# Kernel optimization log

Measured on AMD Instinct MI355X. Metric: run time of the kernel, lower is better.

Reference implementation:

```python
import jax, jax.numpy as jnp
import numpy as np

OUT_H = OUT_W = 15      # POOLER_RESOLUTION (template / pooler_z path)
SCALE = 0.0625          # POOLER_SCALES: 1/16 feature stride
SR = 2                  # POOLER_SAMPLING_RATIO
IMG = 1024.0


def setup_inputs() -> dict:
    key = jax.random.key(0)
    k1, k2, k3, k4, k5 = jax.random.split(key, 5)
    x = jax.random.normal(k1, (2, 256, 64, 64), dtype=jnp.float32)
    N = 512
    cx = jax.random.uniform(k2, (N,), minval=32.0, maxval=IMG - 32.0)
    cy = jax.random.uniform(k3, (N,), minval=32.0, maxval=IMG - 32.0)
    wh = jax.random.uniform(k4, (N, 2), minval=32.0, maxval=160.0)
    x1 = jnp.clip(cx - wh[:, 0] / 2, 0.0, IMG - 1)
    x2 = jnp.clip(cx + wh[:, 0] / 2, 0.0, IMG - 1)
    y1 = jnp.clip(cy - wh[:, 1] / 2, 0.0, IMG - 1)
    y2 = jnp.clip(cy + wh[:, 1] / 2, 0.0, IMG - 1)
    boxes = jnp.stack([x1, y1, x2, y2], axis=1).astype(jnp.float32)
    batch_idx = jax.random.randint(k5, (N,), 0, 2, dtype=jnp.int32)
    return {"x": x, "boxes": boxes, "batch_idx": batch_idx}


def _axis_idx(p, size):
    """ROIAlign bilinear index/frac/validity along one axis. p: [N, K] float."""
    valid = (p >= -1.0) & (p <= size)
    p = jnp.clip(p, 0.0, size - 1.0)
    lo = jnp.floor(p).astype(jnp.int32)
    lo = jnp.minimum(lo, size - 1)
    hi = jnp.minimum(lo + 1, size - 1)
    frac = p - lo.astype(p.dtype)  # 0 when lo==size-1 (matches torch clamp)
    return lo, hi, frac, valid


def roi_align(feats, boxes, batch_idx, out_h, out_w, scale, sr):
    B, C, H, W = feats.shape
    b = boxes * scale
    x1, y1, x2, y2 = b[:, 0], b[:, 1], b[:, 2], b[:, 3]
    roi_w = jnp.maximum(x2 - x1, 1.0)
    roi_h = jnp.maximum(y2 - y1, 1.0)
    bin_w = roi_w / out_w
    bin_h = roi_h / out_h
    # sample point k along an axis: start + (k + 0.5)/sr * bin  (k = ph*sr + iy)
    ky = (jnp.arange(out_h * sr, dtype=feats.dtype) + 0.5) / sr
    kx = (jnp.arange(out_w * sr, dtype=feats.dtype) + 0.5) / sr
    ys = y1[:, None] + ky[None, :] * bin_h[:, None]  # [N, out_h*sr]
    xs = x1[:, None] + kx[None, :] * bin_w[:, None]  # [N, out_w*sr]
    ylo, yhi, fy, vy = _axis_idx(ys, H)
    xlo, xhi, fx, vx = _axis_idx(xs, W)
    bi = batch_idx[:, None, None]

    def gather(yi, xi):
        # feats[b, :, y, x] -> [N, out_h*sr, out_w*sr, C]
        return feats[bi, :, yi[:, :, None], xi[:, None, :]]

    wy_lo = (1.0 - fy) * vy
    wy_hi = fy * vy
    wx_lo = (1.0 - fx) * vx
    wx_hi = fx * vx

    def w2(wy, wx):
        return (wy[:, :, None] * wx[:, None, :])[..., None]  # [N,Hs,Ws,1]

    val = (w2(wy_lo, wx_lo) * gather(ylo, xlo)
           + w2(wy_lo, wx_hi) * gather(ylo, xhi)
           + w2(wy_hi, wx_lo) * gather(yhi, xlo)
           + w2(wy_hi, wx_hi) * gather(yhi, xhi))
    N = boxes.shape[0]
    val = val.reshape(N, out_h, sr, out_w, sr, C).mean(axis=(2, 4))
    return jnp.transpose(val, (0, 3, 1, 2))  # [N, C, out_h, out_w]


def reference(x, boxes, batch_idx):
    # EMMFeatureExtractor.forward with sr=None -> pooler_z (template ROIAlign 15x15)
    return roi_align(x, boxes, batch_idx, OUT_H, OUT_W, SCALE, SR)
```

## Files before the change

kernel.cpp:

```cpp
#include <hip/hip_runtime.h>

constexpr int NROI = 512;
constexpr int CCH  = 256;
constexpr int HH   = 64;
constexpr int WWd  = 64;
constexpr int OHh  = 15;
constexpr int OWw  = 15;
constexpr float SCL = 0.0625f;
constexpr int TSTR  = 17;
constexpr int TROWS = 16;
constexpr int CHUNK  = 64;
constexpr int NCHUNK = CCH / CHUNK;

__global__ __launch_bounds__(256, 4)
void roi_align_kernel(const float* __restrict__ x,
                      const float* __restrict__ boxes,
                      const int* __restrict__ bidx,
                      float* __restrict__ out) {
  __shared__ float T[4][TROWS * TSTR];
  __shared__ float wx_s[OWw][3];
  __shared__ float wy_s[OHh][3];
  __shared__ int   jb_s[OWw];
  __shared__ int   rb_s[OHh];

  const int roi = blockIdx.x >> 2;
  const int g   = blockIdx.x & 3;
  const int t   = threadIdx.x;

  if (t < 32) {
    const int axis = t >> 4;
    const int o    = t & 15;
    if (o < OHh) {
      const float p1v = boxes[roi * 4 + axis] * SCL;
      const float p2v = boxes[roi * 4 + 2 + axis] * SCL;
      const float sz  = fmaxf(p2v - p1v, 1.0f);
      const float bin = sz * (1.0f / 15.0f);
      int lo[2]; float wl[2], wh[2];
#pragma unroll
      for (int s = 0; s < 2; ++s) {
        float p = p1v + ((float)(2 * o + s) + 0.5f) * 0.5f * bin;
        const float valid = (p >= -1.0f && p <= 64.0f) ? 0.5f : 0.0f;
        p = fminf(fmaxf(p, 0.0f), 63.0f);
        const int l = (int)p;
        const float f = p - (float)l;
        lo[s] = l; wl[s] = (1.0f - f) * valid; wh[s] = f * valid;
      }
      const int base = min(lo[0], WWd - 3);
      float w[3] = {0.f, 0.f, 0.f};
#pragma unroll
      for (int s = 0; s < 2; ++s) {
        const int hi = min(lo[s] + 1, WWd - 1);
        w[lo[s] - base] += wl[s];
        w[hi - base]    += wh[s];
      }
      if (axis == 0) { jb_s[o] = base; wx_s[o][0] = w[0]; wx_s[o][1] = w[1]; wx_s[o][2] = w[2]; }
      else           { rb_s[o] = base; wy_s[o][0] = w[0]; wy_s[o][1] = w[1]; wy_s[o][2] = w[2]; }
    }
  }
  __syncthreads();

  const int r0 = rb_s[0];
  const int R  = rb_s[OHh - 1] + 3 - r0;
  const int bi = bidx[roi];

  const bool hasA = (t < R * OWw);
  float ax0 = 0.f, ax1 = 0.f, ax2 = 0.f;
  const float* aptr = x;
  int aT = 0;
  if (hasA) {
    const int ar = t / OWw, aw = t - ar * OWw;
    ax0 = wx_s[aw][0]; ax1 = wx_s[aw][1]; ax2 = wx_s[aw][2];
    aptr = x + (((size_t)bi * CCH + g * CHUNK) * HH + (size_t)(r0 + ar)) * WWd + jb_s[aw];
    aT = ar * TSTR + aw;
  }

  const bool hasB = (t < OHh * OWw);
  float by0 = 0.f, by1 = 0.f, by2 = 0.f;
  int bT = 0;
  float* optr = out;
  if (hasB) {
    const int oh = t / OWw;
    by0 = wy_s[oh][0]; by1 = wy_s[oh][1]; by2 = wy_s[oh][2];
    bT = (rb_s[oh] - r0) * TSTR + (t - oh * OWw);
    optr = out + ((size_t)roi * CCH + (size_t)g * CHUNK) * (OHh * OWw) + t;
  }

  constexpr size_t CSTR = (size_t)HH * WWd;
  constexpr int OSTR = OHh * OWw;

  for (int it = 0; it < CHUNK / 2; ++it) {
    float* T0 = T[(it & 1) * 2];
    float* T1 = T[(it & 1) * 2 + 1];
    if (hasA) {
      const float* p0 = aptr;
      const float* p1 = aptr + CSTR;
      const float v0 = fmaf(p0[0], ax0, fmaf(p0[1], ax1, p0[2] * ax2));
      const float v1 = fmaf(p1[0], ax0, fmaf(p1[1], ax1, p1[2] * ax2));
      T0[aT] = v0;
      T1[aT] = v1;
      aptr += 2 * CSTR;
    }
    __syncthreads();
    if (hasB) {
      const float a0 = T0[bT], a1 = T0[bT + TSTR], a2 = T0[bT + 2 * TSTR];
      const float b0 = T1[bT], b1 = T1[bT + TSTR], b2 = T1[bT + 2 * TSTR];
      const float o0 = fmaf(a0, by0, fmaf(a1, by1, a2 * by2));
      const float o1 = fmaf(b0, by0, fmaf(b1, by1, b2 * by2));
      __builtin_nontemporal_store(o0, optr);
      __builtin_nontemporal_store(o1, optr + OSTR);
      optr += 2 * OSTR;
    }
  }
}

extern "C" void kernel_launch(void* const* d_in, const int* in_sizes, int n_in,
                              void* d_out, int out_size, void* d_ws, size_t ws_size,
                              hipStream_t stream) {
  const float* x     = (const float*)d_in[0];
  const float* boxes = (const float*)d_in[1];
  const int*   bid   = (const int*)d_in[2];
  float* out = (float*)d_out;
  hipLaunchKernelGGL(roi_align_kernel, dim3(NROI * NCHUNK), dim3(256), 0, stream,
                     x, boxes, bid, out);
}
```

Baseline: 156.6 us.

## Replace LDS two-stage separable ROIAlign with per-thread 2x2 register tiles

Drops the shared-memory staging and the per-iteration block barrier. Each lane now computes its own axis weights and produces a 2x2 tile of output bins from a 4x4 input window, read with four unaligned float4 loads per channel. The four waves each take 16 channels of the 64-channel chunk. This removes synchronization and LDS traffic but duplicates weight computation per thread. Edge lanes also write the same clamped outputs twice, and the non-temporal store hint is gone.

```diff
diff --git a/kernel.cpp b/kernel.cpp
--- a/kernel.cpp
+++ b/kernel.cpp
@@ -7,109 +7,112 @@
 constexpr int OHh  = 15;
 constexpr int OWw  = 15;
 constexpr float SCL = 0.0625f;
-constexpr int TSTR  = 17;
-constexpr int TROWS = 16;
 constexpr int CHUNK  = 64;
 constexpr int NCHUNK = CCH / CHUNK;
+constexpr int OSTR   = OHh * OWw;
+constexpr size_t CSTR = (size_t)HH * WWd;
+
+typedef float f4 __attribute__((ext_vector_type(4)));
+typedef f4 __attribute__((aligned(4))) f4a;
+
+__device__ __forceinline__ void axis_w(float p1v, float p2v, int o,
+                                       int& base, float& W0, float& W1, float& W2) {
+  const float sz  = fmaxf(p2v - p1v, 1.0f);
+  const float bin = sz * (1.0f / 15.0f);
+  float w0 = 0.f, w1 = 0.f, w2 = 0.f;
+  int l0 = 0;
+#pragma unroll
+  for (int s = 0; s < 2; ++s) {
+    float p = p1v + ((float)(2 * o + s) + 0.5f) * 0.5f * bin;
+    const float valid = (p >= -1.0f && p <= 64.0f) ? 0.5f : 0.0f;
+    p = fminf(fmaxf(p, 0.0f), 63.0f);
+    const int l = (int)p;
+    const float f = p - (float)l;
+    const float wl = (1.0f - f) * valid;
+    const float wh = f * valid;
+    if (s == 0) l0 = min(l, WWd - 3);
+    const int dl = l - l0;
+    const int dh = min(l + 1, WWd - 1) - l0;
+    w0 += (dl == 0) ? wl : 0.f;
+    w1 += (dl == 1) ? wl : 0.f;
+    w2 += (dl == 2) ? wl : 0.f;
+    w0 += (dh == 0) ? wh : 0.f;
+    w1 += (dh == 1) ? wh : 0.f;
+    w2 += (dh == 2) ? wh : 0.f;
+  }
+  base = l0; W0 = w0; W1 = w1; W2 = w2;
+}
+
+__device__ __forceinline__ f4 shift_w(float w0, float w1, float w2, int off) {
+  f4 r;
+  if (off == 0) { r.x = w0;  r.y = w1; r.z = w2; r.w = 0.f; }
+  else          { r.x = 0.f; r.y = w0; r.z = w1; r.w = w2;  }
+  return r;
+}
+
+__device__ __forceinline__ float dot4(f4 a, f4 w) {
+  return fmaf(a.x, w.x, fmaf(a.y, w.y, fmaf(a.z, w.z, a.w * w.w)));
+}
 
 __global__ __launch_bounds__(256, 4)
 void roi_align_kernel(const float* __restrict__ x,
                       const float* __restrict__ boxes,
                       const int* __restrict__ bidx,
                       float* __restrict__ out) {
-  __shared__ float T[4][TROWS * TSTR];
-  __shared__ float wx_s[OWw][3];
-  __shared__ float wy_s[OHh][3];
-  __shared__ int   jb_s[OWw];
-  __shared__ int   rb_s[OHh];
+  const int roi  = blockIdx.x >> 2;
+  const int g    = blockIdx.x & 3;
+  const int t    = threadIdx.x;
+  const int wv   = t >> 6;
+  const int lane = t & 63;
+  const int ohp  = lane >> 3;
+  const int owp  = lane & 7;
+  const int oh0 = min(2 * ohp, OHh - 2), oh1 = oh0 + 1;
+  const int ow0 = min(2 * owp, OWw - 2), ow1 = ow0 + 1;
 
-  const int roi = blockIdx.x >> 2;
-  const int g   = blockIdx.x & 3;
-  const int t   = threadIdx.x;
+  const float bx1 = boxes[roi * 4 + 0] * SCL;
+  const float by1 = boxes[roi * 4 + 1] * SCL;
+  const float bx2 = boxes[roi * 4 + 2] * SCL;
+  const float by2 = boxes[roi * 4 + 3] * SCL;
 
-  if (t < 32) {
-    const int axis = t >> 4;
-    const int o    = t & 15;
-    if (o < OHh) {
-      const float p1v = boxes[roi * 4 + axis] * SCL;
-      const float p2v = boxes[roi * 4 + 2 + axis] * SCL;
-      const float sz  = fmaxf(p2v - p1v, 1.0f);
-      const float bin = sz * (1.0f / 15.0f);
-      int lo[2]; float wl[2], wh[2];
-#pragma unroll
-      for (int s = 0; s < 2; ++s) {
-        float p = p1v + ((float)(2 * o + s) + 0.5f) * 0.5f * bin;
-        const float valid = (p >= -1.0f && p <= 64.0f) ? 0.5f : 0.0f;
-        p = fminf(fmaxf(p, 0.0f), 63.0f);
-        const int l = (int)p;
-        const float f = p - (float)l;
-        lo[s] = l; wl[s] = (1.0f - f) * valid; wh[s] = f * valid;
-      }
-      const int base = min(lo[0], WWd - 3);
-      float w[3] = {0.f, 0.f, 0.f};
-#pragma unroll
-      for (int s = 0; s < 2; ++s) {
-        const int hi = min(lo[s] + 1, WWd - 1);
-        w[lo[s] - base] += wl[s];
-        w[hi - base]    += wh[s];
-      }
-      if (axis == 0) { jb_s[o] = base; wx_s[o][0] = w[0]; wx_s[o][1] = w[1]; wx_s[o][2] = w[2]; }
-      else           { rb_s[o] = base; wy_s[o][0] = w[0]; wy_s[o][1] = w[1]; wy_s[o][2] = w[2]; }
-    }
-  }
-  __syncthreads();
+  int xbA, xbB, ybA, ybB;
+  float a0, a1, a2, b0, b1, b2, c0w, c1w, c2w, d0, d1, d2;
+  axis_w(bx1, bx2, ow0, xbA, a0, a1, a2);
+  axis_w(bx1, bx2, ow1, xbB, b0, b1, b2);
+  axis_w(by1, by2, oh0, ybA, c0w, c1w, c2w);
+  axis_w(by1, by2, oh1, ybB, d0, d1, d2);
 
-  const int r0 = rb_s[0];
-  const int R  = rb_s[OHh - 1] + 3 - r0;
+  const int jw = min(xbA, WWd - 4);
+  const int rw = min(ybA, HH - 4);
+  const f4 WXA = shift_w(a0, a1, a2, xbA - jw);
+  const f4 WXB = shift_w(b0, b1, b2, xbB - jw);
+  const f4 WYA = shift_w(c0w, c1w, c2w, ybA - rw);
+  const f4 WYB = shift_w(d0, d1, d2, ybB - rw);
+
   const int bi = bidx[roi];
+  const int c0 = g * CHUNK + wv * (CHUNK / 4);
+  const float* xp = x + (((size_t)bi * CCH + c0) * HH + rw) * WWd + jw;
+  float* op = out + ((size_t)roi * CCH + c0) * OSTR + oh0 * OWw + ow0;
 
-  const bool hasA = (t < R * OWw);
-  float ax0 = 0.f, ax1 = 0.f, ax2 = 0.f;
-  const float* aptr = x;
-  int aT = 0;
-  if (hasA) {
-    const int ar = t / OWw, aw = t - ar * OWw;
-    ax0 = wx_s[aw][0]; ax1 = wx_s[aw][1]; ax2 = wx_s[aw][2];
-    aptr = x + (((size_t)bi * CCH + g * CHUNK) * HH + (size_t)(r0 + ar)) * WWd + jb_s[aw];
-    aT = ar * TSTR + aw;
-  }
-
-  const bool hasB = (t < OHh * OWw);
-  float by0 = 0.f, by1 = 0.f, by2 = 0.f;
-  int bT = 0;
-  float* optr = out;
-  if (hasB) {
-    const int oh = t / OWw;
-    by0 = wy_s[oh][0]; by1 = wy_s[oh][1]; by2 = wy_s[oh][2];
-    bT = (rb_s[oh] - r0) * TSTR + (t - oh * OWw);
-    optr = out + ((size_t)roi * CCH + (size_t)g * CHUNK) * (OHh * OWw) + t;
-  }
-
-  constexpr size_t CSTR = (size_t)HH * WWd;
-  constexpr int OSTR = OHh * OWw;
-
-  for (int it = 0; it < CHUNK / 2; ++it) {
-    float* T0 = T[(it & 1) * 2];
-    float* T1 = T[(it & 1) * 2 + 1];
-    if (hasA) {
-      const float* p0 = aptr;
-      const float* p1 = aptr + CSTR;
-      const float v0 = fmaf(p0[0], ax0, fmaf(p0[1], ax1, p0[2] * ax2));
-      const float v1 = fmaf(p1[0], ax0, fmaf(p1[1], ax1, p1[2] * ax2));
-      T0[aT] = v0;
-      T1[aT] = v1;
-      aptr += 2 * CSTR;
-    }
-    __syncthreads();
-    if (hasB) {
-      const float a0 = T0[bT], a1 = T0[bT + TSTR], a2 = T0[bT + 2 * TSTR];
-      const float b0 = T1[bT], b1 = T1[bT + TSTR], b2 = T1[bT + 2 * TSTR];
-      const float o0 = fmaf(a0, by0, fmaf(a1, by1, a2 * by2));
-      const float o1 = fmaf(b0, by0, fmaf(b1, by1, b2 * by2));
-      __builtin_nontemporal_store(o0, optr);
-      __builtin_nontemporal_store(o1, optr + OSTR);
-      optr += 2 * OSTR;
-    }
+#pragma unroll 4
+  for (int it = 0; it < CHUNK / 4; ++it) {
+    const f4 r0 = *(const f4a*)(xp);
+    const f4 r1 = *(const f4a*)(xp + WWd);
+    const f4 r2 = *(const f4a*)(xp + 2 * WWd);
+    const f4 r3 = *(const f4a*)(xp + 3 * WWd);
+    const float hA0 = dot4(r0, WXA), hB0 = dot4(r0, WXB);
+    const float hA1 = dot4(r1, WXA), hB1 = dot4(r1, WXB);
+    const float hA2 = dot4(r2, WXA), hB2 = dot4(r2, WXB);
+    const float hA3 = dot4(r3, WXA), hB3 = dot4(r3, WXB);
+    const float oAA = fmaf(hA0, WYA.x, fmaf(hA1, WYA.y, fmaf(hA2, WYA.z, hA3 * WYA.w)));
+    const float oAB = fmaf(hB0, WYA.x, fmaf(hB1, WYA.y, fmaf(hB2, WYA.z, hB3 * WYA.w)));
+    const float oBA = fmaf(hA0, WYB.x, fmaf(hA1, WYB.y, fmaf(hA2, WYB.z, hA3 * WYB.w)));
+    const float oBB = fmaf(hB0, WYB.x, fmaf(hB1, WYB.y, fmaf(hB2, WYB.z, hB3 * WYB.w)));
+    op[0]       = oAA;
+    op[1]       = oAB;
+    op[OWw]     = oBA;
+    op[OWw + 1] = oBB;
+    xp += CSTR;
+    op += OSTR;
   }
 }
 
```

After: 152.2 us. 1.03x faster.
